# Performance work log

Measured on AMD Instinct MI355X. Metric: run time of the kernel, lower is better.

Reference implementation:

```python
import jax, jax.numpy as jnp
import numpy as np

N, F_IN, F_OUT = 8192, 512, 256
ALPHA = 0.2          # LeakyReLU negative slope
NEG_BIG = -9e15      # mask value from the original module


def setup_inputs() -> dict:
    key = jax.random.key(0)
    k1, k2, k3, k4, k5 = jax.random.split(key, 5)
    x = jax.random.normal(k1, (N, F_IN), dtype=jnp.float32)
    adj = jax.random.randint(k2, (N, N), 0, 2, dtype=jnp.int32)
    # xavier_uniform with gain=1.414
    def xavier(k, shape, gain=1.414):
        fan_in, fan_out = shape[0], shape[1]
        bound = gain * np.sqrt(6.0 / (fan_in + fan_out))
        return jax.random.uniform(k, shape, jnp.float32, -bound, bound)
    W = xavier(k3, (F_IN, F_OUT))
    a1 = xavier(k4, (F_OUT, 1))
    a2 = xavier(k5, (F_OUT, 1))
    return {"x": x, "adj": adj, "W": W, "a1": a1, "a2": a2}


def reference(x, adj, W, a1, a2):
    h = x @ W                                   # [N, F_OUT]
    logit_1 = h @ a1                            # [N, 1]
    logit_2 = h @ a2                            # [N, 1]
    e = jax.nn.leaky_relu(logit_1 + logit_2.T, ALPHA)      # [N, N]
    e = jnp.where(adj > 0, e, jnp.float32(NEG_BIG))
    mean_h = jnp.mean(h, axis=0, keepdims=True)            # [1, F_OUT]
    glob_logit = jax.nn.leaky_relu(logit_1 + mean_h @ a2, ALPHA)  # [N, 1]
    e_all = jnp.concatenate([e, glob_logit], axis=-1)      # [N, N+1]
    attention = jax.nn.softmax(e_all, axis=-1)
    h_all = jnp.concatenate([h, mean_h], axis=0)           # [N+1, F_OUT]
    return jax.nn.elu(attention @ h_all)                   # [N, F_OUT]
```

## Files before the change

### kernel.cpp

```cpp
#include <hip/hip_runtime.h>

#define NROW 8192
#define FIN  512
#define FOUT 256
#define ALPHA 0.2f

typedef float  f32x4  __attribute__((ext_vector_type(4)));
typedef int    i32x4  __attribute__((ext_vector_type(4)));
typedef __bf16 bf16x8 __attribute__((ext_vector_type(8)));
typedef __bf16 bf16x4 __attribute__((ext_vector_type(4)));

__global__ void k1_wt(const float* __restrict__ W, unsigned short* __restrict__ WbT_u) {
    __bf16* WbT = (__bf16*)WbT_u;
    __shared__ float tw[32][33];
    int bx = blockIdx.x & 7;
    int by = blockIdx.x >> 3;
    int f0 = bx * 32, k0 = by * 32;
    int tx = threadIdx.x & 31, ty = threadIdx.x >> 5;
#pragma unroll
    for (int r = 0; r < 4; ++r)
        tw[ty + 8*r][tx] = W[(k0 + ty + 8*r) * FOUT + f0 + tx];
    __syncthreads();
#pragma unroll
    for (int r = 0; r < 4; ++r)
        WbT[(f0 + ty + 8*r) * FIN + k0 + tx] = (__bf16)tw[tx][ty + 8*r];
}

__global__ __launch_bounds__(256, 2) void k2_gemm1(const float* __restrict__ x,
                                                   const unsigned short* __restrict__ WbT_u,
                                                   unsigned short* __restrict__ hTb_u) {
    const __bf16* WbT = (const __bf16*)WbT_u;
    __bf16* hTb = (__bf16*)hTb_u;
    int i0 = blockIdx.x * 32;
    int t = threadIdx.x;
    int lane = t & 63, wv = t >> 6;
    int lm = lane & 15, lg = lane >> 4;
    int wf0 = wv * 64;

    f32x4 acc[4][2];
#pragma unroll
    for (int a = 0; a < 4; ++a)
#pragma unroll
        for (int b = 0; b < 2; ++b) acc[a][b] = (f32x4){0.f, 0.f, 0.f, 0.f};

    for (int kt = 0; kt < FIN; kt += 32) {
        bf16x8 af[4];
#pragma unroll
        for (int fi = 0; fi < 4; ++fi)
            af[fi] = *(const bf16x8*)(WbT + (wf0 + fi*16 + lm) * FIN + kt + lg*8);
        bf16x8 bfr[2];
#pragma unroll
        for (int ii = 0; ii < 2; ++ii) {
            const float* xp = x + (i0 + ii*16 + lm) * FIN + kt + lg*8;
            f32x4 v0 = *(const f32x4*)(xp);
            f32x4 v1 = *(const f32x4*)(xp + 4);
            bf16x8 b;
#pragma unroll
            for (int e = 0; e < 4; ++e) { b[e] = (__bf16)v0[e]; b[4+e] = (__bf16)v1[e]; }
            bfr[ii] = b;
        }
#pragma unroll
        for (int fi = 0; fi < 4; ++fi)
#pragma unroll
            for (int ii = 0; ii < 2; ++ii)
                acc[fi][ii] = __builtin_amdgcn_mfma_f32_16x16x32_bf16(af[fi], bfr[ii], acc[fi][ii], 0, 0, 0);
    }
#pragma unroll
    for (int fi = 0; fi < 4; ++fi)
#pragma unroll
        for (int ii = 0; ii < 2; ++ii)
#pragma unroll
            for (int q = 0; q < 4; ++q)
                hTb[(wf0 + fi*16 + lg*4 + q) * NROW + i0 + ii*16 + lm] = (__bf16)acc[fi][ii][q];
}

__global__ void k3_logits(const unsigned short* __restrict__ hTb_u,
                          const float* __restrict__ a1, const float* __restrict__ a2,
                          float* __restrict__ l1, float* __restrict__ l2) {
    const __bf16* hTb = (const __bf16*)hTb_u;
    int i = blockIdx.x * 256 + threadIdx.x;
    float s1 = 0.f, s2 = 0.f;
    for (int f = 0; f < FOUT; ++f) {
        float h = (float)hTb[f * NROW + i];
        s1 += h * a1[f];
        s2 += h * a2[f];
    }
    l1[i] = s1; l2[i] = s2;
}

__global__ void k3_mean(const unsigned short* __restrict__ hTb_u, float* __restrict__ mean_h) {
    const __bf16* hTb = (const __bf16*)hTb_u;
    int f = blockIdx.x;
    int t = threadIdx.x;
    float s = 0.f;
    for (int i = t; i < NROW; i += 256) s += (float)hTb[f * NROW + i];
#pragma unroll
    for (int m = 1; m < 64; m <<= 1) s += __shfl_xor(s, m);
    __shared__ float red[4];
    if ((t & 63) == 0) red[t >> 6] = s;
    __syncthreads();
    if (t == 0) mean_h[f] = (red[0] + red[1] + red[2] + red[3]) * (1.0f / NROW);
}

__global__ void k3_eg(const float* __restrict__ l1, const float* __restrict__ mean_h,
                      const float* __restrict__ a2, float* __restrict__ eg) {
    __shared__ float red[5];
    int t = threadIdx.x;
    float v = mean_h[t] * a2[t];
#pragma unroll
    for (int m = 1; m < 64; m <<= 1) v += __shfl_xor(v, m);
    if ((t & 63) == 0) red[t >> 6] = v;
    __syncthreads();
    if (t == 0) red[4] = red[0] + red[1] + red[2] + red[3];
    __syncthreads();
    float mda2 = red[4];
    int i = blockIdx.x * 256 + t;
    float g = l1[i] + mda2;
    eg[i] = __expf(fmaxf(g, ALPHA * g));
}

__global__ __launch_bounds__(256, 2) void k4_attn(const int* __restrict__ adj,
                                                  const unsigned short* __restrict__ hTb_u,
                                                  const float* __restrict__ l1,
                                                  const float* __restrict__ l2,
                                                  float* __restrict__ outpT,
                                                  float* __restrict__ Zp,
                                                  int js, int jwidth, int ntiles) {
    const __bf16* hTb = (const __bf16*)hTb_u;
    __shared__ __align__(16) __bf16 wlds[64 * 64];

    int b = blockIdx.x;
    int js_idx = b % js;
    int it = b / js;
    int i0 = it * 64;
    int jstart = js_idx * jwidth;

    int t = threadIdx.x;
    int lane = t & 63, wv = t >> 6;
    int lm = lane & 15, lg = lane >> 4;
    int wf0 = wv * 64;
    int r = t >> 2, cc = t & 3;
    int i_glob = i0 + r;
    float l1v = l1[i_glob];

    const i32x4* adj4 = (const i32x4*)adj;
    const f32x4* l24  = (const f32x4*)l2;
    long arow = (long)i_glob * (NROW / 4);

    f32x4 acc[4][4];
#pragma unroll
    for (int a = 0; a < 4; ++a)
#pragma unroll
        for (int c = 0; c < 4; ++c) acc[a][c] = (f32x4){0.f, 0.f, 0.f, 0.f};
    float zpart = 0.f;

    i32x4 adjA[4], adjB[4];
    f32x4 l2A[4], l2B[4];

    auto loadT = [&](i32x4 (&adjR)[4], f32x4 (&l2R)[4], int jb) {
        int c4 = jb >> 2;
#pragma unroll
        for (int k = 0; k < 4; ++k) {
            adjR[k] = adj4[arow + c4 + cc + 4*k];
            l2R[k]  = l24[c4 + cc + 4*k];
        }
    };

    auto procT = [&](i32x4 (&adjR)[4], f32x4 (&l2R)[4], int jb) {
        bf16x4 pk[4];
        float zadd = 0.f;
#pragma unroll
        for (int k = 0; k < 4; ++k) {
            bf16x4 p;
#pragma unroll
            for (int e = 0; e < 4; ++e) {
                float s = l1v + l2R[k][e];
                float w = (adjR[k][e] > 0) ? __expf(fmaxf(s, ALPHA * s)) : 0.0f;
                __bf16 wb = (__bf16)w;
                p[e] = wb;
                zadd += (float)wb;
            }
            pk[k] = p;
        }
        zpart += zadd;
        __syncthreads();
#pragma unroll
        for (int k = 0; k < 4; ++k) {
            int jl = cc * 4 + 16 * k;
            int blk = jl >> 3;
            int eo = r * 64 + ((blk ^ (r & 7)) << 3) + (jl & 7);
            *(bf16x4*)(wlds + eo) = pk[k];
        }
        __syncthreads();
#pragma unroll
        for (int ks = 0; ks < 2; ++ks) {
            bf16x8 af[4];
#pragma unroll
            for (int fi = 0; fi < 4; ++fi)
                af[fi] = *(const bf16x8*)(hTb + (wf0 + fi*16 + lm) * NROW + jb + ks*32 + lg*8);
            bf16x8 bw[4];
#pragma unroll
            for (int ii = 0; ii < 4; ++ii) {
                int row = ii * 16 + lm;
                int blk = ks * 4 + lg;
                bw[ii] = *(const bf16x8*)(wlds + row * 64 + ((blk ^ (row & 7)) << 3));
            }
#pragma unroll
            for (int fi = 0; fi < 4; ++fi)
#pragma unroll
                for (int ii = 0; ii < 4; ++ii)
                    acc[fi][ii] = __builtin_amdgcn_mfma_f32_16x16x32_bf16(af[fi], bw[ii], acc[fi][ii], 0, 0, 0);
        }
    };

    loadT(adjA, l2A, jstart);
    for (int tt = 0; tt < ntiles; tt += 2) {
        loadT(adjB, l2B, jstart + (tt + 1) * 64);
        procT(adjA, l2A, jstart + tt * 64);
        if (tt + 2 < ntiles) loadT(adjA, l2A, jstart + (tt + 2) * 64);
        procT(adjB, l2B, jstart + (tt + 1) * 64);
    }

    float zs = zpart + __shfl_xor(zpart, 1);
    zs += __shfl_xor(zs, 2);
    if (cc == 0) Zp[js_idx * NROW + i_glob] = zs;

#pragma unroll
    for (int fi = 0; fi < 4; ++fi)
#pragma unroll
        for (int ii = 0; ii < 4; ++ii)
#pragma unroll
            for (int q = 0; q < 4; ++q)
                outpT[js_idx * (NROW * FOUT) + (wf0 + fi*16 + lg*4 + q) * NROW + i0 + ii*16 + lm] = acc[fi][ii][q];
}

__global__ void k5_final(const float* __restrict__ outpT, const float* __restrict__ Zp,
                         const float* __restrict__ eg, const float* __restrict__ mean_h,
                         float* __restrict__ out, int js) {
    __shared__ float tile[64][65];
    int b = blockIdx.x;
    int it = b >> 2, ft = b & 3;
    int i0 = it * 64, f0 = ft * 64;
    int t = threadIdx.x;
    {
        int fl = t >> 2, icb = (t & 3) * 16;
#pragma unroll
        for (int c = 0; c < 4; ++c) {
            f32x4 v = (f32x4){0.f, 0.f, 0.f, 0.f};
            for (int s = 0; s < js; ++s) {
                f32x4 u = *(const f32x4*)(outpT + s * (NROW * FOUT) + (f0 + fl) * NROW + i0 + icb + 4*c);
                v += u;
            }
#pragma unroll
            for (int e = 0; e < 4; ++e) tile[fl][icb + 4*c + e] = v[e];
        }
    }
    __syncthreads();
    int il = t >> 2, fcb = (t & 3) * 16;
    int i = i0 + il;
    float egi = eg[i];
    float z = egi;
    for (int s = 0; s < js; ++s) z += Zp[s * NROW + i];
#pragma unroll
    for (int c = 0; c < 4; ++c) {
        f32x4 o;
#pragma unroll
        for (int e = 0; e < 4; ++e) {
            int fl = fcb + 4*c + e;
            float num = tile[fl][il] + egi * mean_h[f0 + fl];
            float val = num / z;
            o[e] = val > 0.f ? val : (__expf(val) - 1.0f);
        }
        *(f32x4*)(out + (long)i * FOUT + f0 + fcb + 4*c) = o;
    }
}

extern "C" void kernel_launch(void* const* d_in, const int* in_sizes, int n_in,
                              void* d_out, int out_size, void* d_ws, size_t ws_size,
                              hipStream_t stream) {
    const float* x   = (const float*)d_in[0];
    const int*   adj = (const int*)d_in[1];
    const float* W   = (const float*)d_in[2];
    const float* a1  = (const float*)d_in[3];
    const float* a2  = (const float*)d_in[4];
    float* out = (float*)d_out;
    char* ws = (char*)d_ws;

    unsigned short* hTb = (unsigned short*)(ws);
    unsigned short* WbT = (unsigned short*)(ws + 4194304);
    float* l1     = (float*)(ws + 4456448);
    float* l2     = (float*)(ws + 4489216);
    float* eg     = (float*)(ws + 4521984);
    float* mean_h = (float*)(ws + 4554752);
    float* Zp     = (float*)(ws + 4555776);
    float* outpT  = (float*)(ws + 4687872);

    size_t base = 4687872;
    size_t part = (size_t)NROW * FOUT * 4;
    int js = 1;
    if (ws_size >= base + 4 * part) js = 4;
    else if (ws_size >= base + 2 * part) js = 2;
    int jwidth = NROW / js;
    int ntiles = jwidth / 64;

    hipLaunchKernelGGL(k1_wt,     dim3(128),      dim3(256), 0, stream, W, WbT);
    hipLaunchKernelGGL(k2_gemm1,  dim3(256),      dim3(256), 0, stream, x, WbT, hTb);
    hipLaunchKernelGGL(k3_logits, dim3(32),       dim3(256), 0, stream, hTb, a1, a2, l1, l2);
    hipLaunchKernelGGL(k3_mean,   dim3(256),      dim3(256), 0, stream, hTb, mean_h);
    hipLaunchKernelGGL(k3_eg,     dim3(32),       dim3(256), 0, stream, l1, mean_h, a2, eg);
    hipLaunchKernelGGL(k4_attn,   dim3(128 * js), dim3(256), 0, stream, adj, hTb, l1, l2, outpT, Zp, js, jwidth, ntiles);
    hipLaunchKernelGGL(k5_final,  dim3(512),      dim3(256), 0, stream, outpT, Zp, eg, mean_h, out, js);
}
```

Baseline: 182.0 us.

## Double-buffer attention weight tiles in LDS and fold eg kernel into final

The attention kernel now keeps two LDS buffers for the bf16 weight tile, so the next tile's exp/mask staging overlaps the current tile's MFMAs and each tile needs one barrier instead of two. The separate k3_eg launch is removed and its global-logit computation is recomputed inside k5_final. Launch bounds are raised to 3 blocks per CU, and js can reach 8 when the workspace allows, which gives more blocks but makes k5 sum more partial outputs. The extra LDS and register pressure from the higher occupancy target could cause spills.

```diff
diff --git a/kernel.cpp b/kernel.cpp
--- a/kernel.cpp
+++ b/kernel.cpp
@@ -102,24 +102,7 @@
     if (t == 0) mean_h[f] = (red[0] + red[1] + red[2] + red[3]) * (1.0f / NROW);
 }
 
-__global__ void k3_eg(const float* __restrict__ l1, const float* __restrict__ mean_h,
-                      const float* __restrict__ a2, float* __restrict__ eg) {
-    __shared__ float red[5];
-    int t = threadIdx.x;
-    float v = mean_h[t] * a2[t];
-#pragma unroll
-    for (int m = 1; m < 64; m <<= 1) v += __shfl_xor(v, m);
-    if ((t & 63) == 0) red[t >> 6] = v;
-    __syncthreads();
-    if (t == 0) red[4] = red[0] + red[1] + red[2] + red[3];
-    __syncthreads();
-    float mda2 = red[4];
-    int i = blockIdx.x * 256 + t;
-    float g = l1[i] + mda2;
-    eg[i] = __expf(fmaxf(g, ALPHA * g));
-}
-
-__global__ __launch_bounds__(256, 2) void k4_attn(const int* __restrict__ adj,
+__global__ __launch_bounds__(256, 3) void k4_attn(const int* __restrict__ adj,
                                                   const unsigned short* __restrict__ hTb_u,
                                                   const float* __restrict__ l1,
                                                   const float* __restrict__ l2,
@@ -127,7 +110,7 @@
                                                   float* __restrict__ Zp,
                                                   int js, int jwidth, int ntiles) {
     const __bf16* hTb = (const __bf16*)hTb_u;
-    __shared__ __align__(16) __bf16 wlds[64 * 64];
+    __shared__ __align__(16) __bf16 wlds[2][64 * 64];
 
     int b = blockIdx.x;
     int js_idx = b % js;
@@ -155,43 +138,40 @@
     float zpart = 0.f;
 
     i32x4 adjA[4], adjB[4];
-    f32x4 l2A[4], l2B[4];
-
-    auto loadT = [&](i32x4 (&adjR)[4], f32x4 (&l2R)[4], int jb) {
+
+    auto loadT = [&](i32x4 (&adjR)[4], int jb) {
         int c4 = jb >> 2;
 #pragma unroll
+        for (int k = 0; k < 4; ++k)
+            adjR[k] = adj4[arow + c4 + cc + 4*k];
+    };
+
+    auto stageT = [&](int bufi, i32x4 (&adjR)[4], int jb) {
+        int c4 = jb >> 2;
+        __bf16* wl = wlds[bufi];
+        float zadd = 0.f;
+#pragma unroll
         for (int k = 0; k < 4; ++k) {
-            adjR[k] = adj4[arow + c4 + cc + 4*k];
-            l2R[k]  = l24[c4 + cc + 4*k];
-        }
-    };
-
-    auto procT = [&](i32x4 (&adjR)[4], f32x4 (&l2R)[4], int jb) {
-        bf16x4 pk[4];
-        float zadd = 0.f;
-#pragma unroll
-        for (int k = 0; k < 4; ++k) {
+            f32x4 l2v = l24[c4 + cc + 4*k];
             bf16x4 p;
 #pragma unroll
             for (int e = 0; e < 4; ++e) {
-                float s = l1v + l2R[k][e];
+                float s = l1v + l2v[e];
                 float w = (adjR[k][e] > 0) ? __expf(fmaxf(s, ALPHA * s)) : 0.0f;
                 __bf16 wb = (__bf16)w;
                 p[e] = wb;
                 zadd += (float)wb;
             }
-            pk[k] = p;
-        }
-        zpart += zadd;
-        __syncthreads();
-#pragma unroll
-        for (int k = 0; k < 4; ++k) {
             int jl = cc * 4 + 16 * k;
             int blk = jl >> 3;
             int eo = r * 64 + ((blk ^ (r & 7)) << 3) + (jl & 7);
-            *(bf16x4*)(wlds + eo) = pk[k];
-        }
-        __syncthreads();
+            *(bf16x4*)(wl + eo) = p;
+        }
+        zpart += zadd;
+    };
+
+    auto mfmaT = [&](int bufi, int jb) {
+        const __bf16* wl = wlds[bufi];
 #pragma unroll
         for (int ks = 0; ks < 2; ++ks) {
             bf16x8 af[4];
@@ -203,7 +183,7 @@
             for (int ii = 0; ii < 4; ++ii) {
                 int row = ii * 16 + lm;
                 int blk = ks * 4 + lg;
-                bw[ii] = *(const bf16x8*)(wlds + row * 64 + ((blk ^ (row & 7)) << 3));
+                bw[ii] = *(const bf16x8*)(wl + row * 64 + ((blk ^ (row & 7)) << 3));
             }
 #pragma unroll
             for (int fi = 0; fi < 4; ++fi)
@@ -213,12 +193,19 @@
         }
     };
 
-    loadT(adjA, l2A, jstart);
+    loadT(adjA, jstart);
+    stageT(0, adjA, jstart);
+    loadT(adjB, jstart + 64);
+    __syncthreads();
     for (int tt = 0; tt < ntiles; tt += 2) {
-        loadT(adjB, l2B, jstart + (tt + 1) * 64);
-        procT(adjA, l2A, jstart + tt * 64);
-        if (tt + 2 < ntiles) loadT(adjA, l2A, jstart + (tt + 2) * 64);
-        procT(adjB, l2B, jstart + (tt + 1) * 64);
+        stageT(1, adjB, jstart + (tt + 1) * 64);
+        if (tt + 2 < ntiles) loadT(adjA, jstart + (tt + 2) * 64);
+        mfmaT(0, jstart + tt * 64);
+        __syncthreads();
+        if (tt + 2 < ntiles) stageT(0, adjA, jstart + (tt + 2) * 64);
+        if (tt + 3 < ntiles) loadT(adjB, jstart + (tt + 3) * 64);
+        mfmaT(1, jstart + (tt + 1) * 64);
+        __syncthreads();
     }
 
     float zs = zpart + __shfl_xor(zpart, 1);
@@ -235,30 +222,41 @@
 }
 
 __global__ void k5_final(const float* __restrict__ outpT, const float* __restrict__ Zp,
-                         const float* __restrict__ eg, const float* __restrict__ mean_h,
-                         float* __restrict__ out, int js) {
+                         const float* __restrict__ l1, const float* __restrict__ mean_h,
+                         const float* __restrict__ a2, float* __restrict__ out, int js) {
     __shared__ float tile[64][65];
+    __shared__ float red[4];
+    __shared__ float s_mda2;
     int b = blockIdx.x;
     int it = b >> 2, ft = b & 3;
     int i0 = it * 64, f0 = ft * 64;
     int t = threadIdx.x;
+
+    float v = mean_h[t] * a2[t];
+#pragma unroll
+    for (int m = 1; m < 64; m <<= 1) v += __shfl_xor(v, m);
+    if ((t & 63) == 0) red[t >> 6] = v;
+    __syncthreads();
+    if (t == 0) s_mda2 = red[0] + red[1] + red[2] + red[3];
+
     {
         int fl = t >> 2, icb = (t & 3) * 16;
 #pragma unroll
         for (int c = 0; c < 4; ++c) {
-            f32x4 v = (f32x4){0.f, 0.f, 0.f, 0.f};
+            f32x4 vv = (f32x4){0.f, 0.f, 0.f, 0.f};
             for (int s = 0; s < js; ++s) {
-                f32x4 u = *(const f32x4*)(outpT + s * (NROW * FOUT) + (f0 + fl) * NROW + i0 + icb + 4*c);
-                v += u;
+                f32x4 u = *(const f32x4*)(outpT + (long)s * (NROW * FOUT) + (f0 + fl) * NROW + i0 + icb + 4*c);
+                vv += u;
             }
 #pragma unroll
-            for (int e = 0; e < 4; ++e) tile[fl][icb + 4*c + e] = v[e];
+            for (int e = 0; e < 4; ++e) tile[fl][icb + 4*c + e] = vv[e];
         }
     }
     __syncthreads();
     int il = t >> 2, fcb = (t & 3) * 16;
     int i = i0 + il;
-    float egi = eg[i];
+    float g = l1[i] + s_mda2;
+    float egi = __expf(fmaxf(g, ALPHA * g));
     float z = egi;
     for (int s = 0; s < js; ++s) z += Zp[s * NROW + i];
 #pragma unroll
@@ -290,15 +288,15 @@
     unsigned short* WbT = (unsigned short*)(ws + 4194304);
     float* l1     = (float*)(ws + 4456448);
     float* l2     = (float*)(ws + 4489216);
-    float* eg     = (float*)(ws + 4521984);
-    float* mean_h = (float*)(ws + 4554752);
-    float* Zp     = (float*)(ws + 4555776);
-    float* outpT  = (float*)(ws + 4687872);
-
-    size_t base = 4687872;
+    float* mean_h = (float*)(ws + 4521984);
+    float* Zp     = (float*)(ws + 4523008);
+    float* outpT  = (float*)(ws + 4785152);
+
+    size_t base = 4785152;
     size_t part = (size_t)NROW * FOUT * 4;
     int js = 1;
-    if (ws_size >= base + 4 * part) js = 4;
+    if      (ws_size >= base + 8 * part) js = 8;
+    else if (ws_size >= base + 4 * part) js = 4;
     else if (ws_size >= base + 2 * part) js = 2;
     int jwidth = NROW / js;
     int ntiles = jwidth / 64;
@@ -307,7 +305,6 @@
     hipLaunchKernelGGL(k2_gemm1,  dim3(256),      dim3(256), 0, stream, x, WbT, hTb);
     hipLaunchKernelGGL(k3_logits, dim3(32),       dim3(256), 0, stream, hTb, a1, a2, l1, l2);
     hipLaunchKernelGGL(k3_mean,   dim3(256),      dim3(256), 0, stream, hTb, mean_h);
-    hipLaunchKernelGGL(k3_eg,     dim3(32),       dim3(256), 0, stream, l1, mean_h, a2, eg);
     hipLaunchKernelGGL(k4_attn,   dim3(128 * js), dim3(256), 0, stream, adj, hTb, l1, l2, outpT, Zp, js, jwidth, ntiles);
-    hipLaunchKernelGGL(k5_final,  dim3(512),      dim3(256), 0, stream, outpT, Zp, eg, mean_h, out, js);
-}
+    hipLaunchKernelGGL(k5_final,  dim3(512),      dim3(256), 0, stream, outpT, Zp, l1, mean_h, a2, out, js);
+}
```

Result: slower. 282.5 us (+55.2%).
